# Kernel tuning notes

Hardware: AMD Instinct MI355X
Metric: run time of the kernel (lower is better)

## Reference

```python
import jax, jax.numpy as jnp
import numpy as np

# Model dims: H features, N half-state-size, R low-rank, CH output channels, KL kernel length
H, N, R, CH, KL = 512, 64, 1, 1, 4096


def setup_inputs() -> dict:
    key = jax.random.key(0)
    ks = jax.random.split(key, 8)
    log_dt = jax.random.uniform(ks[0], (H,), minval=float(np.log(1e-3)), maxval=float(np.log(1e-1)), dtype=jnp.float32)
    # Hurwitz-like poles: negative real part, HiPPO-like imaginary ladder
    w_re = -0.5 - jax.random.uniform(ks[1], (H, N), dtype=jnp.float32)
    w_im = jnp.broadcast_to(np.float32(np.pi) * jnp.arange(N, dtype=jnp.float32), (H, N))
    B_re = jax.random.normal(ks[2], (1, H, N), dtype=jnp.float32)
    B_im = jax.random.normal(ks[3], (1, H, N), dtype=jnp.float32)
    # small low-rank correction keeps the Woodbury denominator away from zero
    P_re = 0.1 * jax.random.normal(ks[4], (R, H, N), dtype=jnp.float32)
    P_im = 0.1 * jax.random.normal(ks[5], (R, H, N), dtype=jnp.float32)
    C_re = jax.random.normal(ks[6], (CH, H, N), dtype=jnp.float32)
    C_im = jax.random.normal(ks[7], (CH, H, N), dtype=jnp.float32)
    return dict(log_dt=log_dt, w_re=w_re, w_im=w_im, B_re=B_re, B_im=B_im,
                P_re=P_re, P_im=P_im, C_re=C_re, C_im=C_im, L=KL)


def _kernel(log_dt, w_re, w_im, B_re, B_im, P_re, P_im, C_re, C_im, L):
    dt = jnp.exp(log_dt)                                   # (H,)
    w = (w_re + 1j * w_im) * dt[:, None]                   # (H,N) discretized poles w*dt
    B = B_re + 1j * B_im                                   # (1,H,N)
    P = P_re + 1j * P_im                                   # (R,H,N)
    Q = jnp.conj(P)                                        # hurwitz=False path: Q = conj(P)
    C = C_re + 1j * C_im                                   # (CH,H,N)

    Lf = L // 2 + 1
    kk = jnp.arange(Lf)
    omega = jnp.exp((-2j * np.pi) * kk / L)                # FFT roots of unity (complex64)
    den = 1.0 + omega
    # Nyquist node (omega = -1) handled analytically below; guard the division
    safe_den = jnp.where(jnp.abs(den) < 1e-6, jnp.ones_like(den), den)
    z = 2.0 * (1.0 - omega) / safe_den                     # bilinear-transform nodes

    Bc = jnp.concatenate([B, P], axis=0)                   # (1+R,H,N)
    Cc = jnp.concatenate([C, Q], axis=0)                   # (CH+R,H,N)
    v = Bc[:, None] * Cc[None]                             # (1+R,CH+R,H,N)

    # Cauchy kernel: r[a,b,h,l] = sum_n v[a,b,h,n] / (z[l] - w[h,n])
    recip = 1.0 / (z[None, None, :] - w[:, :, None])       # (H,N,Lf)
    r = jnp.einsum('abhn,hnl->abhl', v, recip)             # (1+R,CH+R,H,Lf)
    r = r * dt[None, None, :, None]

    # rank-1 Woodbury correction
    k_f = r[:-1, :-1] - r[:-1, -1:] * r[-1:, :-1] / (1.0 + r[-1:, -1:])
    k_f = k_f * 2.0 / safe_den

    if L % 2 == 0:
        # analytic z -> inf limit at the Nyquist node: dt/2 * sum_n v00
        nyq = 0.5 * dt[None, None, :] * jnp.sum(v[:-1, :-1], axis=-1)  # (1,CH,H)
        k_f = k_f.at[..., -1].set(nyq)

    k = jnp.fft.irfft(k_f, n=L, axis=-1)[..., :L]          # (1,CH,H,L) real
    return k[-1]                                           # (CH,H,L)


def reference(log_dt, w_re, w_im, B_re, B_im, P_re, P_im, C_re, C_im, L):
    return _kernel(log_dt, w_re, w_im, B_re, B_im, P_re, P_im, C_re, C_im, L)
```

## Files before the change

kernel.cpp:

```cpp
#include <hip/hip_runtime.h>
#include <hip/hip_bf16.h>
#include <math.h>


#define HH   512
#define NN   64
#define LLEN 4096
#define MM   2048
#define NTHREADS 1024
#define ZPAD(i) ((i) + ((i) >> 4))

typedef float v2f __attribute__((ext_vector_type(2)));

__device__ __forceinline__ float sinr(float r) { return __builtin_amdgcn_sinf(r); }
__device__ __forceinline__ float cosr(float r) { return __builtin_amdgcn_cosf(r); }
__device__ __forceinline__ float rcpf(float x) { return __builtin_amdgcn_rcpf(x); }

__device__ __forceinline__ void pk_fma_acc(v2f& acc, v2f a, v2f b) {
    asm("v_pk_fma_f32 %0, %1, %2, %0" : "+v"(acc) : "v"(a), "v"(b));
}
__device__ __forceinline__ v2f pk_fma(v2f a, v2f b, v2f c) {
    v2f d; asm("v_pk_fma_f32 %0, %1, %2, %3" : "=v"(d) : "v"(a), "v"(b), "v"(c));
    return d;
}
__device__ __forceinline__ v2f pk_mul(v2f a, v2f b) {
    v2f d; asm("v_pk_mul_f32 %0, %1, %2" : "=v"(d) : "v"(a), "v"(b));
    return d;
}

__global__ __launch_bounds__(NTHREADS, 8) void ssknplr_kernel(
    const float* __restrict__ log_dt,
    const float* __restrict__ w_re, const float* __restrict__ w_im,
    const float* __restrict__ B_re, const float* __restrict__ B_im,
    const float* __restrict__ P_re, const float* __restrict__ P_im,
    const float* __restrict__ C_re, const float* __restrict__ C_im,
    float* __restrict__ out)
{
    __shared__ float4 s_p4[NN][7];
    __shared__ float2 s_Z[ZPAD(MM) + 1];

    const int h   = blockIdx.x;
    const int tid = threadIdx.x;

    if (tid < NN) {
        const int n   = tid;
        const int idx = h * NN + n;
        const float dt = expf(log_dt[h]);
        const float wr = w_re[idx] * dt;
        const float wi = w_im[idx] * dt;
        const float Br = B_re[idx], Bi = B_im[idx];
        const float Pr = P_re[idx], Pi = P_im[idx];
        const float Cr = C_re[idx], Ci = C_im[idx];
        const float v00r = dt * (Br * Cr - Bi * Ci);
        const float v00i = dt * (Br * Ci + Bi * Cr);
        const float v01r = dt * (Br * Pr + Bi * Pi);
        const float v01i = dt * (Bi * Pr - Br * Pi);
        const float v10r = dt * (Pr * Cr - Pi * Ci);
        const float v10i = dt * (Pr * Ci + Pi * Cr);
        const float v11  = dt * (Pr * Pr + Pi * Pi);
        s_p4[n][0] = make_float4(wi, wi, -wr, -wr);
        s_p4[n][1] = make_float4(wr * wr, wr * wr, v00r, v00r);
        s_p4[n][2] = make_float4(v00i, v00i, -v00i, -v00i);
        s_p4[n][3] = make_float4(v01r, v01r, v01i, v01i);
        s_p4[n][4] = make_float4(-v01i, -v01i, v10r, v10r);
        s_p4[n][5] = make_float4(v10i, v10i, -v10i, -v10i);
        s_p4[n][6] = make_float4(v11, v11, 0.0f, 0.0f);
    }
    __syncthreads();

    v2f tv;
    {
        const float rx = (float)tid * (1.0f / 8192.0f);
        const float ry = (float)(tid + 1024) * (1.0f / 8192.0f);
        tv.x = sinr(rx) * rcpf(cosr(rx));
        tv.y = sinr(ry) * rcpf(cosr(ry));
    }
    const v2f neg2 = {-2.0f, -2.0f};

    v2f a00r = {0.f,0.f}, a00i = {0.f,0.f}, a01r = {0.f,0.f}, a01i = {0.f,0.f};
    v2f a10r = {0.f,0.f}, a10i = {0.f,0.f}, a11r = {0.f,0.f}, a11i = {0.f,0.f};

    #pragma unroll 2
    for (int n = 0; n < NN; ++n) {
        const float4 f0 = s_p4[n][0];
        const float4 f1 = s_p4[n][1];
        const float4 f2 = s_p4[n][2];
        const float4 f3 = s_p4[n][3];
        const float4 f4 = s_p4[n][4];
        const float4 f5 = s_p4[n][5];
        const float4 f6 = s_p4[n][6];
        const v2f wiv   = {f0.x, f0.y}, nr    = {f0.z, f0.w};
        const v2f wr2   = {f1.x, f1.y}, v00r  = {f1.z, f1.w};
        const v2f v00i  = {f2.x, f2.y}, nv00i = {f2.z, f2.w};
        const v2f v01r  = {f3.x, f3.y}, v01i  = {f3.z, f3.w};
        const v2f nv01i = {f4.x, f4.y}, v10r  = {f4.z, f4.w};
        const v2f v10i  = {f5.x, f5.y}, nv10i = {f5.z, f5.w};
        const v2f v11   = {f6.x, f6.y};

        const v2f mdim = pk_fma(tv, neg2, wiv);
        const v2f den  = pk_fma(mdim, mdim, wr2);
        const float ip = rcpf(den.x * den.y);
        const v2f ipv  = {ip, ip};
        const v2f dsw  = {den.y, den.x};
        const v2f inv  = pk_mul(dsw, ipv);
        const v2f ur   = pk_mul(nr, inv);
        const v2f ui   = pk_mul(mdim, inv);

        pk_fma_acc(a00r, v00r, ur);  pk_fma_acc(a00r, nv00i, ui);
        pk_fma_acc(a00i, v00r, ui);  pk_fma_acc(a00i, v00i,  ur);
        pk_fma_acc(a01r, v01r, ur);  pk_fma_acc(a01r, nv01i, ui);
        pk_fma_acc(a01i, v01r, ui);  pk_fma_acc(a01i, v01i,  ur);
        pk_fma_acc(a10r, v10r, ur);  pk_fma_acc(a10r, nv10i, ui);
        pk_fma_acc(a10i, v10r, ui);  pk_fma_acc(a10i, v10i,  ur);
        pk_fma_acc(a11r, v11, ur);   pk_fma_acc(a11i, v11,   ui);
    }

    {
        const v2f dr = a11r + 1.0f;
        const v2f di = a11i;
        const v2f dd = __builtin_elementwise_fma(dr, dr, di * di);
        v2f dinv; dinv.x = rcpf(dd.x); dinv.y = rcpf(dd.y);
        const v2f numr = a01r * a10r - a01i * a10i;
        const v2f numi = a01r * a10i + a01i * a10r;
        const v2f cr = (numr * dr + numi * di) * dinv;
        const v2f ci = (numi * dr - numr * di) * dinv;
        const v2f Wr = a00r - cr;
        const v2f Wi = a00i - ci;
        const v2f Kr = __builtin_elementwise_fma(-tv, Wi, Wr);
        const v2f Ki = __builtin_elementwise_fma( tv, Wr, Wi);
        s_Z[ZPAD(tid)] = make_float2(Kr.x, (tid == 0) ? 0.0f : Ki.x);
        s_Z[ZPAD(tid + 1024)] = make_float2(Kr.y, Ki.y);
    }
    if (tid == 0) {
        float sr = 0.f;
        for (int n = 0; n < NN; ++n) sr += s_p4[n][1].z;
        s_Z[ZPAD(MM)] = make_float2(0.5f * sr, 0.0f);
    }
    __syncthreads();

    {
        const int k = tid;
        if (k == 0) {
            const float a = s_Z[ZPAD(0)].x;
            const float b = s_Z[ZPAD(MM)].x;
            s_Z[ZPAD(0)] = make_float2(0.5f * (a + b), 0.5f * (a - b));
            const float2 km = s_Z[ZPAD(MM / 2)];
            s_Z[ZPAD(MM / 2)] = make_float2(km.x, -km.y);
        } else {
            const float2 Ka = s_Z[ZPAD(k)];
            const float2 Kb = s_Z[ZPAD(MM - k)];
            const float rk = (float)k * (1.0f / 4096.0f);
            const float sk = sinr(rk);
            const float ck = cosr(rk);
            const float Pr = 0.5f * (Ka.x + Kb.x), Pi = 0.5f * (Ka.y - Kb.y);
            const float Dr = 0.5f * (Ka.x - Kb.x), Di = 0.5f * (Ka.y + Kb.y);
            const float al = sk * Dr + ck * Di;
            const float be = ck * Dr - sk * Di;
            s_Z[ZPAD(k)]      = make_float2(Pr - al, Pi + be);
            s_Z[ZPAD(MM - k)] = make_float2(Pr + al, be - Pi);
        }
    }
    __syncthreads();

    for (int s = 10; s >= 1; s -= 2) {
        const int H = 1 << s;
        const int Q = H >> 1;
        const float scale = rcpf((float)(2 * H));
        if (tid < 512) {
            const int b    = tid;
            const int j    = b & (Q - 1);
            const int base = ((b >> (s - 1)) << (s + 1)) + j;
            const int i0 = base, i1 = base + Q, i2 = base + H, i3 = base + H + Q;
            const float rev = (float)j * scale;
            const float c  = cosr(rev);
            const float sn = sinr(rev);
            const float wbr = c * c - sn * sn;
            const float wbi = 2.0f * c * sn;
            const float2 u0 = s_Z[ZPAD(i0)];
            const float2 u1 = s_Z[ZPAD(i1)];
            const float2 u2 = s_Z[ZPAD(i2)];
            const float2 u3 = s_Z[ZPAD(i3)];
            const float a0r = u0.x + u2.x, a0i = u0.y + u2.y;
            const float d0r = u0.x - u2.x, d0i = u0.y - u2.y;
            const float a1r = u1.x + u3.x, a1i = u1.y + u3.y;
            const float d1r = u1.x - u3.x, d1i = u1.y - u3.y;
            const float e0r = d0r * c  - d0i * sn, e0i = d0r * sn + d0i * c;
            const float e1r = -(d1r * sn) - d1i * c, e1i = d1r * c - d1i * sn;
            s_Z[ZPAD(i0)] = make_float2(a0r + a1r, a0i + a1i);
            const float t0r = a0r - a1r, t0i = a0i - a1i;
            s_Z[ZPAD(i1)] = make_float2(t0r * wbr - t0i * wbi, t0r * wbi + t0i * wbr);
            s_Z[ZPAD(i2)] = make_float2(e0r + e1r, e0i + e1i);
            const float t1r = e0r - e1r, t1i = e0i - e1i;
            s_Z[ZPAD(i3)] = make_float2(t1r * wbr - t1i * wbi, t1r * wbi + t1i * wbr);
        }
        __syncthreads();
    }
    {
        const int i0 = tid << 1, i1 = i0 | 1;
        const float2 u = s_Z[ZPAD(i0)];
        const float2 v = s_Z[ZPAD(i1)];
        s_Z[ZPAD(i0)] = make_float2(u.x + v.x, u.y + v.y);
        s_Z[ZPAD(i1)] = make_float2(u.x - v.x, u.y - v.y);
    }
    __syncthreads();

    const float scale = 1.0f / (float)MM;
    float2* o2 = (float2*)out + (size_t)h * MM;
    #pragma unroll
    for (int q = 0; q < 2; ++q) {
        const int m = tid + q * NTHREADS;
        const int r = (int)(__brev((unsigned)m) >> 21);
        const float2 z = s_Z[ZPAD(r)];
        o2[m] = make_float2(z.x * scale, z.y * scale);
    }
}

extern "C" void kernel_launch(void* const* d_in, const int* in_sizes, int n_in,
                              void* d_out, int out_size, void* d_ws, size_t ws_size,
                              hipStream_t stream) {
    const float* log_dt = (const float*)d_in[0];
    const float* w_re   = (const float*)d_in[1];
    const float* w_im   = (const float*)d_in[2];
    const float* B_re   = (const float*)d_in[3];
    const float* B_im   = (const float*)d_in[4];
    const float* P_re   = (const float*)d_in[5];
    const float* P_im   = (const float*)d_in[6];
    const float* C_re   = (const float*)d_in[7];
    const float* C_im   = (const float*)d_in[8];
    float* out = (float*)d_out;

    ssknplr_kernel<<<dim3(HH), dim3(NTHREADS), 0, stream>>>(
        log_dt, w_re, w_im, B_re, B_im, P_re, P_im, C_re, C_im, out);
}
```

Measured before the change: 40.91 us.

## Halve block size, give each thread four frequencies, shrink LDS coefficients

Drops the block to 512 threads, and each thread now evaluates two packed frequency pairs (four nodes). Every shared-memory load of pole and residue coefficients therefore feeds twice as much Cauchy arithmetic. Negated coefficient duplicates are removed (five float4 per pole instead of seven), inline-asm packed FMAs give way to compiler builtins, and the FFT stages drop the idle-half guard. The cost is more live registers per thread (16 packed accumulators), fewer resident threads, and half the threads for the post-processing loops.

Measured after the change: 36.62 us. 10.5% less time.

```diff
diff --git a/kernel.cpp b/kernel.cpp
--- a/kernel.cpp
+++ b/kernel.cpp
@@ -7,7 +7,7 @@
 #define NN   64
 #define LLEN 4096
 #define MM   2048
-#define NTHREADS 1024
+#define NTHREADS 512
 #define ZPAD(i) ((i) + ((i) >> 4))
 
 typedef float v2f __attribute__((ext_vector_type(2)));
@@ -16,19 +16,56 @@
 __device__ __forceinline__ float cosr(float r) { return __builtin_amdgcn_cosf(r); }
 __device__ __forceinline__ float rcpf(float x) { return __builtin_amdgcn_rcpf(x); }
 
-__device__ __forceinline__ void pk_fma_acc(v2f& acc, v2f a, v2f b) {
-    asm("v_pk_fma_f32 %0, %1, %2, %0" : "+v"(acc) : "v"(a), "v"(b));
-}
-__device__ __forceinline__ v2f pk_fma(v2f a, v2f b, v2f c) {
-    v2f d; asm("v_pk_fma_f32 %0, %1, %2, %3" : "=v"(d) : "v"(a), "v"(b), "v"(c));
-    return d;
-}
-__device__ __forceinline__ v2f pk_mul(v2f a, v2f b) {
-    v2f d; asm("v_pk_mul_f32 %0, %1, %2" : "=v"(d) : "v"(a), "v"(b));
-    return d;
-}
-
-__global__ __launch_bounds__(NTHREADS, 8) void ssknplr_kernel(
+__device__ __forceinline__ void cauchy_step(
+    const v2f tv, const v2f mwi, const v2f nr, const v2f wr2,
+    const v2f v00r, const v2f v00i, const v2f v01r, const v2f v01i,
+    const v2f v10r, const v2f v10i, const v2f v11,
+    v2f& a00r, v2f& a00i, v2f& a01r, v2f& a01i,
+    v2f& a10r, v2f& a10i, v2f& a11r, v2f& a11i)
+{
+    const v2f dim = __builtin_elementwise_fma(tv, (v2f){2.0f, 2.0f}, mwi);
+    const v2f den = __builtin_elementwise_fma(dim, dim, wr2);
+    const float ip = rcpf(den.x * den.y);
+    v2f inv; inv.x = den.y * ip; inv.y = den.x * ip;
+    const v2f ur = nr * inv;
+    const v2f ui = -(dim * inv);
+    a00r = __builtin_elementwise_fma( v00r, ur, a00r);
+    a00r = __builtin_elementwise_fma(-v00i, ui, a00r);
+    a00i = __builtin_elementwise_fma( v00r, ui, a00i);
+    a00i = __builtin_elementwise_fma( v00i, ur, a00i);
+    a01r = __builtin_elementwise_fma( v01r, ur, a01r);
+    a01r = __builtin_elementwise_fma(-v01i, ui, a01r);
+    a01i = __builtin_elementwise_fma( v01r, ui, a01i);
+    a01i = __builtin_elementwise_fma( v01i, ur, a01i);
+    a10r = __builtin_elementwise_fma( v10r, ur, a10r);
+    a10r = __builtin_elementwise_fma(-v10i, ui, a10r);
+    a10i = __builtin_elementwise_fma( v10r, ui, a10i);
+    a10i = __builtin_elementwise_fma( v10i, ur, a10i);
+    a11r = __builtin_elementwise_fma( v11,  ur, a11r);
+    a11i = __builtin_elementwise_fma( v11,  ui, a11i);
+}
+
+__device__ __forceinline__ void woodbury_K(
+    const v2f tv,
+    const v2f a00r, const v2f a00i, const v2f a01r, const v2f a01i,
+    const v2f a10r, const v2f a10i, const v2f a11r, const v2f a11i,
+    v2f& Kr, v2f& Ki)
+{
+    const v2f dr = a11r + 1.0f;
+    const v2f di = a11i;
+    const v2f dd = __builtin_elementwise_fma(dr, dr, di * di);
+    v2f dinv; dinv.x = rcpf(dd.x); dinv.y = rcpf(dd.y);
+    const v2f numr = a01r * a10r - a01i * a10i;
+    const v2f numi = a01r * a10i + a01i * a10r;
+    const v2f cr = (numr * dr + numi * di) * dinv;
+    const v2f ci = (numi * dr - numr * di) * dinv;
+    const v2f Wr = a00r - cr;
+    const v2f Wi = a00i - ci;
+    Kr = __builtin_elementwise_fma(-tv, Wi, Wr);
+    Ki = __builtin_elementwise_fma( tv, Wr, Wi);
+}
+
+__global__ __launch_bounds__(NTHREADS, 4) void ssknplr_kernel(
     const float* __restrict__ log_dt,
     const float* __restrict__ w_re, const float* __restrict__ w_im,
     const float* __restrict__ B_re, const float* __restrict__ B_im,
@@ -36,7 +73,7 @@
     const float* __restrict__ C_re, const float* __restrict__ C_im,
     float* __restrict__ out)
 {
-    __shared__ float4 s_p4[NN][7];
+    __shared__ float4 s_p4[NN][5];
     __shared__ float2 s_Z[ZPAD(MM) + 1];
 
     const int h   = blockIdx.x;
@@ -58,78 +95,59 @@
         const float v10r = dt * (Pr * Cr - Pi * Ci);
         const float v10i = dt * (Pr * Ci + Pi * Cr);
         const float v11  = dt * (Pr * Pr + Pi * Pi);
-        s_p4[n][0] = make_float4(wi, wi, -wr, -wr);
+        s_p4[n][0] = make_float4(-wi, -wi, -wr, -wr);
         s_p4[n][1] = make_float4(wr * wr, wr * wr, v00r, v00r);
-        s_p4[n][2] = make_float4(v00i, v00i, -v00i, -v00i);
-        s_p4[n][3] = make_float4(v01r, v01r, v01i, v01i);
-        s_p4[n][4] = make_float4(-v01i, -v01i, v10r, v10r);
-        s_p4[n][5] = make_float4(v10i, v10i, -v10i, -v10i);
-        s_p4[n][6] = make_float4(v11, v11, 0.0f, 0.0f);
-    }
-    __syncthreads();
-
-    v2f tv;
-    {
-        const float rx = (float)tid * (1.0f / 8192.0f);
-        const float ry = (float)(tid + 1024) * (1.0f / 8192.0f);
-        tv.x = sinr(rx) * rcpf(cosr(rx));
-        tv.y = sinr(ry) * rcpf(cosr(ry));
-    }
-    const v2f neg2 = {-2.0f, -2.0f};
-
-    v2f a00r = {0.f,0.f}, a00i = {0.f,0.f}, a01r = {0.f,0.f}, a01i = {0.f,0.f};
-    v2f a10r = {0.f,0.f}, a10i = {0.f,0.f}, a11r = {0.f,0.f}, a11i = {0.f,0.f};
-
-    #pragma unroll 2
+        s_p4[n][2] = make_float4(v00i, v00i, v01r, v01r);
+        s_p4[n][3] = make_float4(v01i, v01i, v10r, v10r);
+        s_p4[n][4] = make_float4(v10i, v10i, v11, v11);
+    }
+    __syncthreads();
+
+    v2f tvA, tvB;
+    {
+        const float rA0 = (float)tid           * (1.0f / 8192.0f);
+        const float rA1 = (float)(tid + 1024)  * (1.0f / 8192.0f);
+        const float rB0 = (float)(tid + 512)   * (1.0f / 8192.0f);
+        const float rB1 = (float)(tid + 1536)  * (1.0f / 8192.0f);
+        tvA.x = sinr(rA0) * rcpf(cosr(rA0));
+        tvA.y = sinr(rA1) * rcpf(cosr(rA1));
+        tvB.x = sinr(rB0) * rcpf(cosr(rB0));
+        tvB.y = sinr(rB1) * rcpf(cosr(rB1));
+    }
+
+    v2f A00r = {0.f,0.f}, A00i = {0.f,0.f}, A01r = {0.f,0.f}, A01i = {0.f,0.f};
+    v2f A10r = {0.f,0.f}, A10i = {0.f,0.f}, A11r = {0.f,0.f}, A11i = {0.f,0.f};
+    v2f B00r = {0.f,0.f}, B00i = {0.f,0.f}, B01r = {0.f,0.f}, B01i = {0.f,0.f};
+    v2f B10r = {0.f,0.f}, B10i = {0.f,0.f}, B11r = {0.f,0.f}, B11i = {0.f,0.f};
+
     for (int n = 0; n < NN; ++n) {
         const float4 f0 = s_p4[n][0];
         const float4 f1 = s_p4[n][1];
         const float4 f2 = s_p4[n][2];
         const float4 f3 = s_p4[n][3];
         const float4 f4 = s_p4[n][4];
-        const float4 f5 = s_p4[n][5];
-        const float4 f6 = s_p4[n][6];
-        const v2f wiv   = {f0.x, f0.y}, nr    = {f0.z, f0.w};
-        const v2f wr2   = {f1.x, f1.y}, v00r  = {f1.z, f1.w};
-        const v2f v00i  = {f2.x, f2.y}, nv00i = {f2.z, f2.w};
-        const v2f v01r  = {f3.x, f3.y}, v01i  = {f3.z, f3.w};
-        const v2f nv01i = {f4.x, f4.y}, v10r  = {f4.z, f4.w};
-        const v2f v10i  = {f5.x, f5.y}, nv10i = {f5.z, f5.w};
-        const v2f v11   = {f6.x, f6.y};
-
-        const v2f mdim = pk_fma(tv, neg2, wiv);
-        const v2f den  = pk_fma(mdim, mdim, wr2);
-        const float ip = rcpf(den.x * den.y);
-        const v2f ipv  = {ip, ip};
-        const v2f dsw  = {den.y, den.x};
-        const v2f inv  = pk_mul(dsw, ipv);
-        const v2f ur   = pk_mul(nr, inv);
-        const v2f ui   = pk_mul(mdim, inv);
-
-        pk_fma_acc(a00r, v00r, ur);  pk_fma_acc(a00r, nv00i, ui);
-        pk_fma_acc(a00i, v00r, ui);  pk_fma_acc(a00i, v00i,  ur);
-        pk_fma_acc(a01r, v01r, ur);  pk_fma_acc(a01r, nv01i, ui);
-        pk_fma_acc(a01i, v01r, ui);  pk_fma_acc(a01i, v01i,  ur);
-        pk_fma_acc(a10r, v10r, ur);  pk_fma_acc(a10r, nv10i, ui);
-        pk_fma_acc(a10i, v10r, ui);  pk_fma_acc(a10i, v10i,  ur);
-        pk_fma_acc(a11r, v11, ur);   pk_fma_acc(a11i, v11,   ui);
-    }
-
-    {
-        const v2f dr = a11r + 1.0f;
-        const v2f di = a11i;
-        const v2f dd = __builtin_elementwise_fma(dr, dr, di * di);
-        v2f dinv; dinv.x = rcpf(dd.x); dinv.y = rcpf(dd.y);
-        const v2f numr = a01r * a10r - a01i * a10i;
-        const v2f numi = a01r * a10i + a01i * a10r;
-        const v2f cr = (numr * dr + numi * di) * dinv;
-        const v2f ci = (numi * dr - numr * di) * dinv;
-        const v2f Wr = a00r - cr;
-        const v2f Wi = a00i - ci;
-        const v2f Kr = __builtin_elementwise_fma(-tv, Wi, Wr);
-        const v2f Ki = __builtin_elementwise_fma( tv, Wr, Wi);
-        s_Z[ZPAD(tid)] = make_float2(Kr.x, (tid == 0) ? 0.0f : Ki.x);
+        const v2f mwi  = {f0.x, f0.y}, nr   = {f0.z, f0.w};
+        const v2f wr2  = {f1.x, f1.y}, v00r = {f1.z, f1.w};
+        const v2f v00i = {f2.x, f2.y}, v01r = {f2.z, f2.w};
+        const v2f v01i = {f3.x, f3.y}, v10r = {f3.z, f3.w};
+        const v2f v10i = {f4.x, f4.y}, v11  = {f4.z, f4.w};
+        cauchy_step(tvA, mwi, nr, wr2, v00r, v00i, v01r, v01i, v10r, v10i, v11,
+                    A00r, A00i, A01r, A01i, A10r, A10i, A11r, A11i);
+        cauchy_step(tvB, mwi, nr, wr2, v00r, v00i, v01r, v01i, v10r, v10i, v11,
+                    B00r, B00i, B01r, B01i, B10r, B10i, B11r, B11i);
+    }
+
+    {
+        v2f Kr, Ki;
+        woodbury_K(tvA, A00r, A00i, A01r, A01i, A10r, A10i, A11r, A11i, Kr, Ki);
+        s_Z[ZPAD(tid)]        = make_float2(Kr.x, (tid == 0) ? 0.0f : Ki.x);
         s_Z[ZPAD(tid + 1024)] = make_float2(Kr.y, Ki.y);
+    }
+    {
+        v2f Kr, Ki;
+        woodbury_K(tvB, B00r, B00i, B01r, B01i, B10r, B10i, B11r, B11i, Kr, Ki);
+        s_Z[ZPAD(tid + 512)]  = make_float2(Kr.x, Ki.x);
+        s_Z[ZPAD(tid + 1536)] = make_float2(Kr.y, Ki.y);
     }
     if (tid == 0) {
         float sr = 0.f;
@@ -138,8 +156,9 @@
     }
     __syncthreads();
 
-    {
-        const int k = tid;
+    #pragma unroll
+    for (int q = 0; q < 2; ++q) {
+        const int k = tid + (q << 9);
         if (k == 0) {
             const float a = s_Z[ZPAD(0)].x;
             const float b = s_Z[ZPAD(MM)].x;
@@ -166,7 +185,7 @@
         const int H = 1 << s;
         const int Q = H >> 1;
         const float scale = rcpf((float)(2 * H));
-        if (tid < 512) {
+        {
             const int b    = tid;
             const int j    = b & (Q - 1);
             const int base = ((b >> (s - 1)) << (s + 1)) + j;
@@ -196,19 +215,23 @@
         __syncthreads();
     }
     {
-        const int i0 = tid << 1, i1 = i0 | 1;
-        const float2 u = s_Z[ZPAD(i0)];
-        const float2 v = s_Z[ZPAD(i1)];
-        s_Z[ZPAD(i0)] = make_float2(u.x + v.x, u.y + v.y);
-        s_Z[ZPAD(i1)] = make_float2(u.x - v.x, u.y - v.y);
+        #pragma unroll
+        for (int q = 0; q < 2; ++q) {
+            const int b  = tid + (q << 9);
+            const int i0 = b << 1, i1 = i0 | 1;
+            const float2 u = s_Z[ZPAD(i0)];
+            const float2 v = s_Z[ZPAD(i1)];
+            s_Z[ZPAD(i0)] = make_float2(u.x + v.x, u.y + v.y);
+            s_Z[ZPAD(i1)] = make_float2(u.x - v.x, u.y - v.y);
+        }
     }
     __syncthreads();
 
     const float scale = 1.0f / (float)MM;
     float2* o2 = (float2*)out + (size_t)h * MM;
     #pragma unroll
-    for (int q = 0; q < 2; ++q) {
-        const int m = tid + q * NTHREADS;
+    for (int q = 0; q < 4; ++q) {
+        const int m = tid + (q << 9);
         const int r = (int)(__brev((unsigned)m) >> 21);
         const float2 z = s_Z[ZPAD(r)];
         o2[m] = make_float2(z.x * scale, z.y * scale);
```
